# Kernel tuning notes

Hardware: AMD Instinct MI355X
Metric: run time of the kernel (lower is better)

## Reference

```python
import jax, jax.numpy as jnp
import numpy as np

# Dims
B, S, D = 2, 2048, 1024
H, KV = 16, 4            # rosa heads / kv heads -> n_rep = 4
QKB, VB = 16, 32          # query-key bits / value bits
N_REP = H // KV
TAU = 1.0


def setup_inputs() -> dict:
    key = jax.random.key(0)
    ks = jax.random.split(key, 8)
    sc = lambda fan_in: 1.0 / np.sqrt(fan_in)
    return {
        "hidden_states": jax.random.normal(ks[0], (B, S, D), jnp.float32),
        # Linear weights stored (in, out) so y = x @ W
        "Wq": jax.random.normal(ks[1], (D, H * QKB), jnp.float32) * sc(D),
        "Wk": jax.random.normal(ks[2], (D, KV * QKB), jnp.float32) * sc(D),
        "Wv": jax.random.normal(ks[3], (D, KV * VB), jnp.float32) * sc(D),
        "Wo": jax.random.normal(ks[4], (H * VB, D), jnp.float32) * sc(H * VB),
        "v_emb0": jnp.full((H * VB,), -1e-05, jnp.float32),
        "v_emb1": jnp.full((H * VB,), +1e-05, jnp.float32),
    }


def _repeat_kv(x, n_rep):
    # x: [B, KV, S, d] -> [B, KV*n_rep, S, d]
    b, kv, s, d = x.shape
    return jnp.broadcast_to(x[:, :, None], (b, kv, n_rep, s, d)).reshape(b, kv * n_rep, s, d)


def reference(hidden_states, Wq, Wk, Wv, Wo, v_emb0, v_emb1):
    b, s, _ = hidden_states.shape
    q = (hidden_states @ Wq).reshape(b, s, H, QKB).transpose(0, 2, 1, 3)   # [B,H,S,QKB]
    k = (hidden_states @ Wk).reshape(b, s, KV, QKB).transpose(0, 2, 1, 3)
    v = (hidden_states @ Wv).reshape(b, s, KV, VB).transpose(0, 2, 1, 3)
    k = _repeat_kv(k, N_REP)                                               # [B,H,S,QKB]
    v = _repeat_kv(v, N_REP)                                               # [B,H,S,VB]

    # Soft binarization (hard path uses (x > 0); soft path relaxes with sigmoid(x/tau)).
    pq = jax.nn.sigmoid(q / TAU)
    pk = jax.nn.sigmoid(k / TAU)
    pv = jax.nn.sigmoid(v / TAU)

    # Expected number of matching bits between soft-binary q_i and k_j:
    # sum_b [ pq*pk + (1-pq)(1-pk) ] = QKB - sum(pq) - sum(pk) + 2 * pq.pk
    dot = jnp.einsum("bhsd,bhtd->bhst", pq, pk)                            # [B,H,S,S]
    scores = QKB - pq.sum(-1)[:, :, :, None] - pk.sum(-1)[:, :, None, :] + 2.0 * dot

    causal = jnp.tril(jnp.ones((s, s), bool))                              # [S,S]
    scores = jnp.where(causal[None, None], scores, jnp.finfo(scores.dtype).min)
    attn = jax.nn.softmax(scores / TAU, axis=-1)

    vh = jnp.einsum("bhst,bhtd->bhsd", attn, pv)                           # [B,H,S,VB]
    e0 = v_emb0.reshape(1, H, 1, VB)
    e1 = v_emb1.reshape(1, H, 1, VB)
    out = e0 * (1.0 - vh) + e1 * vh                                        # [B,H,S,VB]
    out = out.transpose(0, 2, 1, 3).reshape(b, s, H * VB)
    return out @ Wo                                                        # [B,S,D]
```

## Files before the change

kernel.cpp:

```cpp
#include <hip/hip_runtime.h>
#include <hip/hip_bf16.h>

#define B_    2
#define S_    2048
#define D_    1024
#define H_    16
#define KV_   4
#define QKB_  16
#define VB_   32
#define NTOK  (B_ * S_)
#define L2E_  1.44269504088896f

typedef __attribute__((ext_vector_type(8))) short bshort8;
typedef __attribute__((ext_vector_type(4))) float f32x4;

__device__ __forceinline__ unsigned short bf16_rne(float x) {
    unsigned u = __float_as_uint(x);
    return (unsigned short)((u + 0x7FFFu + ((u >> 16) & 1u)) >> 16);
}
__device__ __forceinline__ unsigned bf16x2_rne(float lo, float hi) {
    return (unsigned)bf16_rne(lo) | ((unsigned)bf16_rne(hi) << 16);
}
__device__ __forceinline__ unsigned cvt_pk_bf16(float lo, float hi) {
    unsigned r;
    asm("v_cvt_pk_bf16_f32 %0, %1, %2" : "=v"(r) : "v"(lo), "v"(hi));
    return r;
}
__device__ __forceinline__ float sum2bf(unsigned u) {
    return __uint_as_float(u << 16) + __uint_as_float(u & 0xFFFF0000u);
}
__device__ __forceinline__ void stage16(const unsigned short* g, unsigned short* l) {
    __builtin_amdgcn_global_load_lds(
        (const __attribute__((address_space(1))) void*)g,
        (__attribute__((address_space(3))) void*)l, 16, 0, 0);
}

__global__ __launch_bounds__(256) void prep_kernel(
    const float* __restrict__ hs,
    const float* __restrict__ Wq, const float* __restrict__ Wk,
    const float* __restrict__ Wv, const float* __restrict__ Wo,
    unsigned short* __restrict__ hs_b,
    unsigned short* __restrict__ Wcat_t, unsigned short* __restrict__ Wot)
{
    __shared__ float T[64][65];
    const int t = threadIdx.x;
    if (blockIdx.x < 2048) {
        int i = blockIdx.x * 256 + t;
        const float4* s = (const float4*)hs;
        float4 a = s[2 * i], b = s[2 * i + 1];
        uint4 o;
        o.x = bf16x2_rne(a.x, a.y); o.y = bf16x2_rne(a.z, a.w);
        o.z = bf16x2_rne(b.x, b.y); o.w = bf16x2_rne(b.z, b.w);
        ((uint4*)hs_b)[i] = o;
        return;
    }
    const int bid = blockIdx.x - 2048;
    const float* src; unsigned short* dst; int K, N, tk, tn, drow0;
    if (bid < 64)       { src = Wq; dst = Wcat_t; K = 1024; N = 256;  int r = bid;       tk = r & 15; tn = r >> 4; drow0 = 0; }
    else if (bid < 80)  { src = Wk; dst = Wcat_t; K = 1024; N = 64;   int r = bid - 64;  tk = r;      tn = 0;      drow0 = 256; }
    else if (bid < 112) { src = Wv; dst = Wcat_t; K = 1024; N = 128;  int r = bid - 80;  tk = r & 15; tn = r >> 4; drow0 = 320; }
    else                { src = Wo; dst = Wot;    K = 512;  N = 1024; int r = bid - 112; tk = r & 7;  tn = r >> 3; drow0 = 0; }
    const int k0 = tk * 64, n0 = tn * 64;
    const int rr = t >> 4, cc = (t & 15) * 4;
    #pragma unroll
    for (int i = 0; i < 4; ++i) {
        float4 v = *(const float4*)(src + (k0 + rr + i * 16) * N + n0 + cc);
        T[rr + i * 16][cc + 0] = v.x; T[rr + i * 16][cc + 1] = v.y;
        T[rr + i * 16][cc + 2] = v.z; T[rr + i * 16][cc + 3] = v.w;
    }
    __syncthreads();
    const int nloc = t >> 2, kc = (t & 3) * 16;
    unsigned o[8];
    #pragma unroll
    for (int j = 0; j < 8; ++j)
        o[j] = bf16x2_rne(T[kc + 2 * j][nloc], T[kc + 2 * j + 1][nloc]);
    unsigned short* dp = dst + (drow0 + n0 + nloc) * K + k0 + kc;
    uint4 w0; w0.x = o[0]; w0.y = o[1]; w0.z = o[2]; w0.w = o[3];
    uint4 w1; w1.x = o[4]; w1.y = o[5]; w1.z = o[6]; w1.w = o[7];
    *(uint4*)(dp) = w0;
    *(uint4*)(dp + 8) = w1;
}

__global__ __launch_bounds__(256, 4) void proj_gemm(
    const unsigned short* __restrict__ Ab, const unsigned short* __restrict__ Btb,
    unsigned short* __restrict__ qg, unsigned short* __restrict__ pko,
    unsigned short* __restrict__ pvT)
{
    __shared__ unsigned short As[64 * 64];
    __shared__ unsigned short Bs[64 * 64];
    const int tid = threadIdx.x, l = tid & 63, w = tid >> 6;
    const int l15 = l & 15, quad = l >> 4;
    const int m0 = blockIdx.x * 64, n0 = blockIdx.y * 64;
    const int sr8 = l >> 3, sc8 = l & 7;
    f32x4 c[4];
    #pragma unroll
    for (int j = 0; j < 4; ++j) c[j] = (f32x4){0.f, 0.f, 0.f, 0.f};

    for (int k0 = 0; k0 < 1024; k0 += 64) {
        int R0 = w * 8, r0 = R0 + sr8;
        int R1 = 32 + w * 8, r1 = R1 + sr8;
        stage16(Ab  + (m0 + r0) * 1024 + k0 + (sc8 ^ (r0 & 7)) * 8, &As[R0 * 64]);
        stage16(Ab  + (m0 + r1) * 1024 + k0 + (sc8 ^ (r1 & 7)) * 8, &As[R1 * 64]);
        stage16(Btb + (n0 + r0) * 1024 + k0 + (sc8 ^ (r0 & 7)) * 8, &Bs[R0 * 64]);
        stage16(Btb + (n0 + r1) * 1024 + k0 + (sc8 ^ (r1 & 7)) * 8, &Bs[R1 * 64]);
        __syncthreads();
        #pragma unroll
        for (int kh = 0; kh < 2; ++kh) {
            const int arow = w * 16 + l15;
            bshort8 a = *(const bshort8*)&As[arow * 64 + (((kh * 4 + quad) ^ (arow & 7)) * 8)];
            #pragma unroll
            for (int bc = 0; bc < 4; ++bc) {
                const int brow = bc * 16 + l15;
                bshort8 b = *(const bshort8*)&Bs[brow * 64 + (((kh * 4 + quad) ^ (brow & 7)) * 8)];
                c[bc] = __builtin_amdgcn_mfma_f32_16x16x32_bf16(a, b, c[bc], 0, 0, 0);
            }
        }
        __syncthreads();
    }

    const int tok0 = m0 + w * 16 + quad * 4;
    #pragma unroll
    for (int bc = 0; bc < 4; ++bc) {
        f32x4 v = c[bc];
        const int n = n0 + bc * 16 + l15;
        float sg[4];
        #pragma unroll
        for (int r = 0; r < 4; ++r)
            sg[r] = 1.f / (1.f + exp2f(-v[r] * L2E_));
        if (n < 256) {
            const int hh = n >> 4, d = n & 15;
            #pragma unroll
            for (int r = 0; r < 4; ++r) {
                int tok = tok0 + r, bb = tok >> 11, ss = tok & 2047;
                qg[(((bb * 16 + hh) * 2048) + ss) * 16 + d] =
                    bf16_rne(L2E_ * (2.f * sg[r] - 1.f));
            }
        } else if (n < 320) {
            const int j = n - 256, kvv = j >> 4, d = j & 15;
            #pragma unroll
            for (int r = 0; r < 4; ++r) {
                int tok = tok0 + r, bb = tok >> 11, ss = tok & 2047;
                pko[(((bb * 4 + kvv) * 2048) + ss) * 16 + d] = bf16_rne(sg[r]);
            }
        } else {
            const int j = n - 320, kvv = j >> 5, d = j & 31;
            const int bb = tok0 >> 11, ss = tok0 & 2047;
            const int tl = ss >> 6, ccol = ss & 63;
            uint2 wv; wv.x = bf16x2_rne(sg[0], sg[1]); wv.y = bf16x2_rne(sg[2], sg[3]);
            *(uint2*)(pvT + ((((bb * 4 + kvv) * 32) + tl) * 32 + d) * 64 + ccol) = wv;
        }
    }
}

__global__ __launch_bounds__(256, 2) void outproj_gemm(
    const unsigned short* __restrict__ Ab, const unsigned short* __restrict__ Btb,
    float* __restrict__ out)
{
    __shared__ unsigned short As[64 * 64];
    __shared__ unsigned short Bs[128 * 64];
    const int tid = threadIdx.x, l = tid & 63, w = tid >> 6;
    const int l15 = l & 15, quad = l >> 4;
    const int m0 = blockIdx.x * 64, n0 = blockIdx.y * 128;
    const int wr = w & 1, wc = w >> 1;
    const int sr8 = l >> 3, sc8 = l & 7;
    f32x4 c[2][4];
    #pragma unroll
    for (int i = 0; i < 2; ++i)
        #pragma unroll
        for (int j = 0; j < 4; ++j) c[i][j] = (f32x4){0.f, 0.f, 0.f, 0.f};

    for (int k0 = 0; k0 < 512; k0 += 64) {
        #pragma unroll
        for (int j = 0; j < 2; ++j) {
            int R = w * 16 + j * 8, r = R + sr8;
            stage16(Ab + (m0 + r) * 512 + k0 + (sc8 ^ (r & 7)) * 8, &As[R * 64]);
        }
        #pragma unroll
        for (int j = 0; j < 4; ++j) {
            int R = j * 32 + w * 8, r = R + sr8;
            stage16(Btb + (n0 + r) * 512 + k0 + (sc8 ^ (r & 7)) * 8, &Bs[R * 64]);
        }
        __syncthreads();
        #pragma unroll
        for (int kh = 0; kh < 2; ++kh) {
            bshort8 a[2], b[4];
            #pragma unroll
            for (int ar = 0; ar < 2; ++ar) {
                int row = wr * 32 + ar * 16 + l15;
                a[ar] = *(const bshort8*)&As[row * 64 + (((kh * 4 + quad) ^ (row & 7)) * 8)];
            }
            #pragma unroll
            for (int bc = 0; bc < 4; ++bc) {
                int row = wc * 64 + bc * 16 + l15;
                b[bc] = *(const bshort8*)&Bs[row * 64 + (((kh * 4 + quad) ^ (row & 7)) * 8)];
            }
            #pragma unroll
            for (int ar = 0; ar < 2; ++ar)
                #pragma unroll
                for (int bc = 0; bc < 4; ++bc)
                    c[ar][bc] = __builtin_amdgcn_mfma_f32_16x16x32_bf16(a[ar], b[bc], c[ar][bc], 0, 0, 0);
        }
        __syncthreads();
    }

    #pragma unroll
    for (int ar = 0; ar < 2; ++ar)
        #pragma unroll
        for (int bc = 0; bc < 4; ++bc) {
            f32x4 v = c[ar][bc];
            const int col = n0 + wc * 64 + bc * 16 + l15;
            const int r0 = m0 + wr * 32 + ar * 16 + quad * 4;
            #pragma unroll
            for (int r = 0; r < 4; ++r)
                out[(r0 + r) * D_ + col] = v[r];
        }
}

#define TILEPASS(QF, A0, A1, LS, DG, QLANE, T0) do {                           \
    f32x4 s0_, s1_, s2_, s3_;                                                  \
    {                                                                          \
        bshort8 kf0_, kf1_, kf2_, kf3_;                                        \
        if (quad < 2) {                                                        \
            kf0_ = *(const bshort8*)&Ks[cur][0 * 256 + koff];                  \
            kf1_ = *(const bshort8*)&Ks[cur][1 * 256 + koff];                  \
            kf2_ = *(const bshort8*)&Ks[cur][2 * 256 + koff];                  \
            kf3_ = *(const bshort8*)&Ks[cur][3 * 256 + koff];                  \
        } else if (quad == 2) { kf0_ = kone; kf1_ = kone; kf2_ = kone; kf3_ = kone; } \
        else                  { kf0_ = zero8; kf1_ = zero8; kf2_ = zero8; kf3_ = zero8; } \
        s0_ = __builtin_amdgcn_mfma_f32_16x16x32_bf16(kf0_, QF, zero4, 0, 0, 0); \
        s1_ = __builtin_amdgcn_mfma_f32_16x16x32_bf16(kf1_, QF, zero4, 0, 0, 0); \
        s2_ = __builtin_amdgcn_mfma_f32_16x16x32_bf16(kf2_, QF, zero4, 0, 0, 0); \
        s3_ = __builtin_amdgcn_mfma_f32_16x16x32_bf16(kf3_, QF, zero4, 0, 0, 0); \
    }                                                                          \
    if (!(DG)) {                                                               \
        PACK4(s0_, 0, LS); PACK4(s1_, 1, LS); PACK4(s2_, 2, LS); PACK4(s3_, 3, LS); \
    } else {                                                                   \
        DPACK4(s0_, 0, LS, QLANE, T0); DPACK4(s1_, 1, LS, QLANE, T0);          \
        DPACK4(s2_, 2, LS, QLANE, T0); DPACK4(s3_, 3, LS, QLANE, T0);          \
    }                                                                          \
    {                                                                          \
        bshort8 pf0_ = *(const bshort8*)&P[wq][l15][quad * 8];                 \
        bshort8 pf1_ = *(const bshort8*)&P[wq][l15][32 + quad * 8];            \
        bshort8 v0_ = *(const bshort8*)&Vs[cur][vrow + vx0];                   \
        bshort8 v1_ = *(const bshort8*)&Vs[cur][vrow + vx1];                   \
        bshort8 v2_ = *(const bshort8*)&Vs[cur][vrow + 1024 + vx0];            \
        bshort8 v3_ = *(const bshort8*)&Vs[cur][vrow + 1024 + vx1];            \
        A0 = __builtin_amdgcn_mfma_f32_16x16x32_bf16(v0_, pf0_, A0, 0, 0, 0);  \
        A1 = __builtin_amdgcn_mfma_f32_16x16x32_bf16(v2_, pf0_, A1, 0, 0, 0);  \
        A0 = __builtin_amdgcn_mfma_f32_16x16x32_bf16(v1_, pf1_, A0, 0, 0, 0);  \
        A1 = __builtin_amdgcn_mfma_f32_16x16x32_bf16(v3_, pf1_, A1, 0, 0, 0);  \
    }                                                                          \
} while (0)

#define PACK4(scv, KS, LS) do {                                                \
    float p0_ = exp2f(scv[0]), p1_ = exp2f(scv[1]);                            \
    float p2_ = exp2f(scv[2]), p3_ = exp2f(scv[3]);                            \
    LS += p0_ + p1_ + p2_ + p3_;                                               \
    uint2 wv_; wv_.x = cvt_pk_bf16(p0_, p1_); wv_.y = cvt_pk_bf16(p2_, p3_);   \
    *(uint2*)&P[wq][l15][(KS) * 16 + quad * 4] = wv_;                          \
} while (0)

#define DPACK4(scv, KS, LS, QLANE, T0) do {                                    \
    float p0_ = ((T0) + (KS) * 16 + quad * 4 + 0 <= (QLANE)) ? exp2f(scv[0]) : 0.f; \
    float p1_ = ((T0) + (KS) * 16 + quad * 4 + 1 <= (QLANE)) ? exp2f(scv[1]) : 0.f; \
    float p2_ = ((T0) + (KS) * 16 + quad * 4 + 2 <= (QLANE)) ? exp2f(scv[2]) : 0.f; \
    float p3_ = ((T0) + (KS) * 16 + quad * 4 + 3 <= (QLANE)) ? exp2f(scv[3]) : 0.f; \
    LS += p0_ + p1_ + p2_ + p3_;                                               \
    uint2 wv_; wv_.x = cvt_pk_bf16(p0_, p1_); wv_.y = cvt_pk_bf16(p2_, p3_);   \
    *(uint2*)&P[wq][l15][(KS) * 16 + quad * 4] = wv_;                          \
} while (0)

#define WRITEOUT(QT, A0, A1, LS) do {                                          \
    float ls_ = LS;                                                            \
    ls_ += __shfl_xor(ls_, 16);                                                \
    ls_ += __shfl_xor(ls_, 32);                                                \
    const float inv_ = 1.f / ls_;                                              \
    const int tok_ = b * 2048 + (QT) * 64 + wq * 16 + l15;                     \
    float o0_[4], o1_[4];                                                      \
    _Pragma("unroll")                                                          \
    for (int r = 0; r < 4; ++r) {                                              \
        o0_[r] = e0v[r]     + dEv[r]     * (A0[r] * inv_);                     \
        o1_[r] = e0v[4 + r] + dEv[4 + r] * (A1[r] * inv_);                     \
    }                                                                          \
    uint2 w0_, w1_;                                                            \
    w0_.x = cvt_pk_bf16(o0_[0], o0_[1]); w0_.y = cvt_pk_bf16(o0_[2], o0_[3]);  \
    w1_.x = cvt_pk_bf16(o1_[0], o1_[1]); w1_.y = cvt_pk_bf16(o1_[2], o1_[3]);  \
    *(uint2*)(xo + tok_ * 512 + h * 32 + quad * 4)      = w0_;                 \
    *(uint2*)(xo + tok_ * 512 + h * 32 + 16 + quad * 4) = w1_;                 \
} while (0)

__global__ __launch_bounds__(256, 2) void attn_kernel(
    const unsigned short* __restrict__ qg_g, const unsigned short* __restrict__ pk_g,
    const unsigned short* __restrict__ pvT_g, const float* __restrict__ e0,
    const float* __restrict__ e1, unsigned short* __restrict__ xo)
{
    __shared__ unsigned short Ks[2][64 * 16];
    __shared__ unsigned short Vs[2][32 * 64];
    __shared__ unsigned short P[4][16][88];
    const int tid = threadIdx.x, l = tid & 63, wq = tid >> 6;
    const int l15 = l & 15, quad = l >> 4;
    const int g = blockIdx.x;
    const int bh = g & 31, p = g >> 5;
    const int qtA = p, qtB = 31 - p;
    const int b = bh >> 4, h = bh & 15, kv = h >> 2;
    const unsigned short* pkb = pk_g + ((b * 4 + kv) * 2048) * 16;
    const unsigned short* pvb = pvT_g + (b * 4 + kv) * 65536;
    const unsigned short* qgb = qg_g + ((b * 16 + h) * 2048) * 16;

    const f32x4 zero4 = {0.f, 0.f, 0.f, 0.f};
    const bshort8 zero8 = {0, 0, 0, 0, 0, 0, 0, 0};
    bshort8 kone = zero8; kone[0] = (short)0x3F80;

    bshort8 qfragA = zero8, qfragB = zero8;
    {
        const unsigned short* qrow = qgb + (qtA * 64 + wq * 16 + l15) * 16;
        uint4 qu0 = *(const uint4*)qrow;
        uint4 qu1 = *(const uint4*)(qrow + 8);
        float s = sum2bf(qu0.x) + sum2bf(qu0.y) + sum2bf(qu0.z) + sum2bf(qu0.w)
                + sum2bf(qu1.x) + sum2bf(qu1.y) + sum2bf(qu1.z) + sum2bf(qu1.w);
        if (quad == 0)      qfragA = __builtin_bit_cast(bshort8, qu0);
        else if (quad == 1) qfragA = __builtin_bit_cast(bshort8, qu1);
        else if (quad == 2) qfragA[0] = (short)bf16_rne(-8.f * L2E_ - 0.5f * s);
    }
    {
        const unsigned short* qrow = qgb + (qtB * 64 + wq * 16 + l15) * 16;
        uint4 qu0 = *(const uint4*)qrow;
        uint4 qu1 = *(const uint4*)(qrow + 8);
        float s = sum2bf(qu0.x) + sum2bf(qu0.y) + sum2bf(qu0.z) + sum2bf(qu0.w)
                + sum2bf(qu1.x) + sum2bf(qu1.y) + sum2bf(qu1.z) + sum2bf(qu1.w);
        if (quad == 0)      qfragB = __builtin_bit_cast(bshort8, qu0);
        else if (quad == 1) qfragB = __builtin_bit_cast(bshort8, qu1);
        else if (quad == 2) qfragB[0] = (short)bf16_rne(-8.f * L2E_ - 0.5f * s);
    }

    f32x4 accA0 = zero4, accA1 = zero4, accB0 = zero4, accB1 = zero4;
    float lsumA = 0.f, lsumB = 0.f;

    const int vrow_s = tid >> 3;
    const unsigned short* vsrc = pvb + vrow_s * 64 + (((tid & 7) ^ (vrow_s & 7)) * 8);
    const unsigned short* ksrc = pkb + (tid >> 1) * 16 + (tid & 1) * 8;

    const int koff = l15 * 16 + quad * 8;
    const int vx0 = ((quad ^ (l15 & 7)) * 8);
    const int vx1 = (((quad + 4) ^ (l15 & 7)) * 8);
    const int vrow = l15 * 64;

    const int qlaneA = qtA * 64 + wq * 16 + l15;
    const int qlaneB = qtB * 64 + wq * 16 + l15;

    stage16(vsrc, &Vs[0][tid * 8]);
    if (tid < 128) stage16(ksrc, &Ks[0][tid * 8]);
    __syncthreads();

    int cur = 0;
    for (int t = 0; t <= qtB; ++t) {
        if (t < qtB) {
            stage16(vsrc + (t + 1) * 2048, &Vs[cur ^ 1][tid * 8]);
            if (tid < 128) stage16(ksrc + (t + 1) * 1024, &Ks[cur ^ 1][tid * 8]);
        }
        TILEPASS(qfragB, accB0, accB1, lsumB, t == qtB, qlaneB, t * 64);
        if (t <= qtA)
            TILEPASS(qfragA, accA0, accA1, lsumA, t == qtA, qlaneA, t * 64);
        __syncthreads();
        cur ^= 1;
    }

    float e0v[8], dEv[8];
    #pragma unroll
    for (int vs = 0; vs < 2; ++vs)
        #pragma unroll
        for (int r = 0; r < 4; ++r) {
            int idx2 = h * 32 + vs * 16 + quad * 4 + r;
            float a = e0[idx2];
            e0v[vs * 4 + r] = a; dEv[vs * 4 + r] = e1[idx2] - a;
        }
    WRITEOUT(qtA, accA0, accA1, lsumA);
    WRITEOUT(qtB, accB0, accB1, lsumB);
}

extern "C" void kernel_launch(void* const* d_in, const int* in_sizes, int n_in,
                              void* d_out, int out_size, void* d_ws, size_t ws_size,
                              hipStream_t stream)
{
    const float* hs = (const float*)d_in[0];
    const float* Wq = (const float*)d_in[1];
    const float* Wk = (const float*)d_in[2];
    const float* Wv = (const float*)d_in[3];
    const float* Wo = (const float*)d_in[4];
    const float* e0 = (const float*)d_in[5];
    const float* e1 = (const float*)d_in[6];
    float* out = (float*)d_out;

    char* ws = (char*)d_ws;
    unsigned short* hs_b   = (unsigned short*)(ws);
    unsigned short* xo     = (unsigned short*)(ws);
    unsigned short* Wcat_t = (unsigned short*)(ws + 8388608);
    unsigned short* Wot    = (unsigned short*)(ws + 8388608 + 917504);
    unsigned short* qg     = (unsigned short*)(ws + 10354688);
    unsigned short* pk     = (unsigned short*)(ws + 12451840);
    unsigned short* pvT    = (unsigned short*)(ws + 12976128);

    prep_kernel<<<2288, 256, 0, stream>>>(hs, Wq, Wk, Wv, Wo, hs_b, Wcat_t, Wot);
    proj_gemm<<<dim3(64, 7), 256, 0, stream>>>(hs_b, Wcat_t, qg, pk, pvT);
    attn_kernel<<<512, 256, 0, stream>>>(qg, pk, pvT, e0, e1, xo);
    outproj_gemm<<<dim3(64, 8), 256, 0, stream>>>(xo, Wot, out);
}
```

Measured before the change: 135.5 us.

## Process two KV tiles per barrier with doubled LDS staging buffers

The attention loop now stages two 64-key K/V tiles per iteration into double-buffered shared memory and runs up to four tile passes between barriers, halving the number of __syncthreads calls. The P scratch buffer gets a per-slot dimension so the two tiles of a step don't overwrite each other. The cost is twice the LDS footprint per block (about 34 KB), which may limit occupancy under the two-blocks-per-CU launch bound, plus larger prefetch bursts.

```diff
diff --git a/kernel.cpp b/kernel.cpp
--- a/kernel.cpp
+++ b/kernel.cpp
@@ -216,15 +216,33 @@
         }
 }
 
-#define TILEPASS(QF, A0, A1, LS, DG, QLANE, T0) do {                           \
+#define PACK4(scv, KS, LS, PS) do {                                            \
+    float p0_ = exp2f(scv[0]), p1_ = exp2f(scv[1]);                            \
+    float p2_ = exp2f(scv[2]), p3_ = exp2f(scv[3]);                            \
+    LS += p0_ + p1_ + p2_ + p3_;                                               \
+    uint2 wv_; wv_.x = cvt_pk_bf16(p0_, p1_); wv_.y = cvt_pk_bf16(p2_, p3_);   \
+    *(uint2*)&P[PS][wq][l15][(KS) * 16 + quad * 4] = wv_;                      \
+} while (0)
+
+#define DPACK4(scv, KS, LS, PS, QLANE, T0) do {                                \
+    float p0_ = ((T0) + (KS) * 16 + quad * 4 + 0 <= (QLANE)) ? exp2f(scv[0]) : 0.f; \
+    float p1_ = ((T0) + (KS) * 16 + quad * 4 + 1 <= (QLANE)) ? exp2f(scv[1]) : 0.f; \
+    float p2_ = ((T0) + (KS) * 16 + quad * 4 + 2 <= (QLANE)) ? exp2f(scv[2]) : 0.f; \
+    float p3_ = ((T0) + (KS) * 16 + quad * 4 + 3 <= (QLANE)) ? exp2f(scv[3]) : 0.f; \
+    LS += p0_ + p1_ + p2_ + p3_;                                               \
+    uint2 wv_; wv_.x = cvt_pk_bf16(p0_, p1_); wv_.y = cvt_pk_bf16(p2_, p3_);   \
+    *(uint2*)&P[PS][wq][l15][(KS) * 16 + quad * 4] = wv_;                      \
+} while (0)
+
+#define TILEPASS(QF, A0, A1, LS, DG, QLANE, T0, TS) do {                       \
     f32x4 s0_, s1_, s2_, s3_;                                                  \
     {                                                                          \
         bshort8 kf0_, kf1_, kf2_, kf3_;                                        \
         if (quad < 2) {                                                        \
-            kf0_ = *(const bshort8*)&Ks[cur][0 * 256 + koff];                  \
-            kf1_ = *(const bshort8*)&Ks[cur][1 * 256 + koff];                  \
-            kf2_ = *(const bshort8*)&Ks[cur][2 * 256 + koff];                  \
-            kf3_ = *(const bshort8*)&Ks[cur][3 * 256 + koff];                  \
+            kf0_ = *(const bshort8*)&Ks[cur][TS][0 * 256 + koff];              \
+            kf1_ = *(const bshort8*)&Ks[cur][TS][1 * 256 + koff];              \
+            kf2_ = *(const bshort8*)&Ks[cur][TS][2 * 256 + koff];              \
+            kf3_ = *(const bshort8*)&Ks[cur][TS][3 * 256 + koff];              \
         } else if (quad == 2) { kf0_ = kone; kf1_ = kone; kf2_ = kone; kf3_ = kone; } \
         else                  { kf0_ = zero8; kf1_ = zero8; kf2_ = zero8; kf3_ = zero8; } \
         s0_ = __builtin_amdgcn_mfma_f32_16x16x32_bf16(kf0_, QF, zero4, 0, 0, 0); \
@@ -233,41 +251,24 @@
         s3_ = __builtin_amdgcn_mfma_f32_16x16x32_bf16(kf3_, QF, zero4, 0, 0, 0); \
     }                                                                          \
     if (!(DG)) {                                                               \
-        PACK4(s0_, 0, LS); PACK4(s1_, 1, LS); PACK4(s2_, 2, LS); PACK4(s3_, 3, LS); \
+        PACK4(s0_, 0, LS, TS); PACK4(s1_, 1, LS, TS);                          \
+        PACK4(s2_, 2, LS, TS); PACK4(s3_, 3, LS, TS);                          \
     } else {                                                                   \
-        DPACK4(s0_, 0, LS, QLANE, T0); DPACK4(s1_, 1, LS, QLANE, T0);          \
-        DPACK4(s2_, 2, LS, QLANE, T0); DPACK4(s3_, 3, LS, QLANE, T0);          \
+        DPACK4(s0_, 0, LS, TS, QLANE, T0); DPACK4(s1_, 1, LS, TS, QLANE, T0);  \
+        DPACK4(s2_, 2, LS, TS, QLANE, T0); DPACK4(s3_, 3, LS, TS, QLANE, T0);  \
     }                                                                          \
     {                                                                          \
-        bshort8 pf0_ = *(const bshort8*)&P[wq][l15][quad * 8];                 \
-        bshort8 pf1_ = *(const bshort8*)&P[wq][l15][32 + quad * 8];            \
-        bshort8 v0_ = *(const bshort8*)&Vs[cur][vrow + vx0];                   \
-        bshort8 v1_ = *(const bshort8*)&Vs[cur][vrow + vx1];                   \
-        bshort8 v2_ = *(const bshort8*)&Vs[cur][vrow + 1024 + vx0];            \
-        bshort8 v3_ = *(const bshort8*)&Vs[cur][vrow + 1024 + vx1];            \
+        bshort8 pf0_ = *(const bshort8*)&P[TS][wq][l15][quad * 8];             \
+        bshort8 pf1_ = *(const bshort8*)&P[TS][wq][l15][32 + quad * 8];        \
+        bshort8 v0_ = *(const bshort8*)&Vs[cur][TS][vrow + vx0];               \
+        bshort8 v1_ = *(const bshort8*)&Vs[cur][TS][vrow + vx1];               \
+        bshort8 v2_ = *(const bshort8*)&Vs[cur][TS][vrow + 1024 + vx0];        \
+        bshort8 v3_ = *(const bshort8*)&Vs[cur][TS][vrow + 1024 + vx1];        \
         A0 = __builtin_amdgcn_mfma_f32_16x16x32_bf16(v0_, pf0_, A0, 0, 0, 0);  \
         A1 = __builtin_amdgcn_mfma_f32_16x16x32_bf16(v2_, pf0_, A1, 0, 0, 0);  \
         A0 = __builtin_amdgcn_mfma_f32_16x16x32_bf16(v1_, pf1_, A0, 0, 0, 0);  \
         A1 = __builtin_amdgcn_mfma_f32_16x16x32_bf16(v3_, pf1_, A1, 0, 0, 0);  \
     }                                                                          \
-} while (0)
-
-#define PACK4(scv, KS, LS) do {                                                \
-    float p0_ = exp2f(scv[0]), p1_ = exp2f(scv[1]);                            \
-    float p2_ = exp2f(scv[2]), p3_ = exp2f(scv[3]);                            \
-    LS += p0_ + p1_ + p2_ + p3_;                                               \
-    uint2 wv_; wv_.x = cvt_pk_bf16(p0_, p1_); wv_.y = cvt_pk_bf16(p2_, p3_);   \
-    *(uint2*)&P[wq][l15][(KS) * 16 + quad * 4] = wv_;                          \
-} while (0)
-
-#define DPACK4(scv, KS, LS, QLANE, T0) do {                                    \
-    float p0_ = ((T0) + (KS) * 16 + quad * 4 + 0 <= (QLANE)) ? exp2f(scv[0]) : 0.f; \
-    float p1_ = ((T0) + (KS) * 16 + quad * 4 + 1 <= (QLANE)) ? exp2f(scv[1]) : 0.f; \
-    float p2_ = ((T0) + (KS) * 16 + quad * 4 + 2 <= (QLANE)) ? exp2f(scv[2]) : 0.f; \
-    float p3_ = ((T0) + (KS) * 16 + quad * 4 + 3 <= (QLANE)) ? exp2f(scv[3]) : 0.f; \
-    LS += p0_ + p1_ + p2_ + p3_;                                               \
-    uint2 wv_; wv_.x = cvt_pk_bf16(p0_, p1_); wv_.y = cvt_pk_bf16(p2_, p3_);   \
-    *(uint2*)&P[wq][l15][(KS) * 16 + quad * 4] = wv_;                          \
 } while (0)
 
 #define WRITEOUT(QT, A0, A1, LS) do {                                          \
@@ -294,9 +295,9 @@
     const unsigned short* __restrict__ pvT_g, const float* __restrict__ e0,
     const float* __restrict__ e1, unsigned short* __restrict__ xo)
 {
-    __shared__ unsigned short Ks[2][64 * 16];
-    __shared__ unsigned short Vs[2][32 * 64];
-    __shared__ unsigned short P[4][16][88];
+    __shared__ unsigned short Ks[2][2][64 * 16];
+    __shared__ unsigned short Vs[2][2][32 * 64];
+    __shared__ unsigned short P[2][4][16][88];
     const int tid = threadIdx.x, l = tid & 63, wq = tid >> 6;
     const int l15 = l & 15, quad = l >> 4;
     const int g = blockIdx.x;
@@ -338,7 +339,8 @@
 
     const int vrow_s = tid >> 3;
     const unsigned short* vsrc = pvb + vrow_s * 64 + (((tid & 7) ^ (vrow_s & 7)) * 8);
-    const unsigned short* ksrc = pkb + (tid >> 1) * 16 + (tid & 1) * 8;
+    const int ktid = tid & 127, kslot = tid >> 7;
+    const unsigned short* ksrc = pkb + (ktid >> 1) * 16 + (ktid & 1) * 8;
 
     const int koff = l15 * 16 + quad * 8;
     const int vx0 = ((quad ^ (l15 & 7)) * 8);
@@ -348,19 +350,29 @@
     const int qlaneA = qtA * 64 + wq * 16 + l15;
     const int qlaneB = qtB * 64 + wq * 16 + l15;
 
-    stage16(vsrc, &Vs[0][tid * 8]);
-    if (tid < 128) stage16(ksrc, &Ks[0][tid * 8]);
+    stage16(vsrc, &Vs[0][0][tid * 8]);
+    stage16(vsrc + 2048, &Vs[0][1][tid * 8]);
+    stage16(ksrc + kslot * 1024, &Ks[0][kslot][ktid * 8]);
     __syncthreads();
 
     int cur = 0;
-    for (int t = 0; t <= qtB; ++t) {
-        if (t < qtB) {
-            stage16(vsrc + (t + 1) * 2048, &Vs[cur ^ 1][tid * 8]);
-            if (tid < 128) stage16(ksrc + (t + 1) * 1024, &Ks[cur ^ 1][tid * 8]);
-        }
-        TILEPASS(qfragB, accB0, accB1, lsumB, t == qtB, qlaneB, t * 64);
-        if (t <= qtA)
-            TILEPASS(qfragA, accA0, accA1, lsumA, t == qtA, qlaneA, t * 64);
+    for (int tt = 0; tt <= qtB; tt += 2) {
+        if (tt + 2 <= qtB) {
+            const int ns = cur ^ 1;
+            const int n1 = (tt + 3 <= qtB) ? tt + 3 : qtB;
+            stage16(vsrc + (tt + 2) * 2048, &Vs[ns][0][tid * 8]);
+            stage16(vsrc + n1 * 2048, &Vs[ns][1][tid * 8]);
+            const int kt = (tt + 2 + kslot <= qtB) ? tt + 2 + kslot : qtB;
+            stage16(ksrc + kt * 1024, &Ks[ns][kslot][ktid * 8]);
+        }
+        const int t0 = tt, t1 = tt + 1;
+        TILEPASS(qfragB, accB0, accB1, lsumB, t0 == qtB, qlaneB, t0 * 64, 0);
+        if (t1 <= qtB)
+            TILEPASS(qfragB, accB0, accB1, lsumB, t1 == qtB, qlaneB, t1 * 64, 1);
+        if (t0 <= qtA)
+            TILEPASS(qfragA, accA0, accA1, lsumA, t0 == qtA, qlaneA, t0 * 64, 0);
+        if (t1 <= qtA)
+            TILEPASS(qfragA, accA0, accA1, lsumA, t1 == qtA, qlaneA, t1 * 64, 1);
         __syncthreads();
         cur ^= 1;
     }
```

Result: no change. 135.6 us (+0.1%).
